# Kernel optimization log

Measured on AMD Instinct MI355X. Metric: run time of the kernel, lower is better.

The kernel has to match this reference:

```python
import jax, jax.numpy as jnp
import numpy as np

B, IN_CAPS, IN_DIM = 64, 2048, 16
NUM_CAPS, DIM_CAPS = 32, 16
NUM_ROUTING = 3
EPS = 1e-7


def squash(s):
    # squash along last (capsule vector) dim: ||s||^2/(1+||s||^2) * s/||s||
    sq_norm = jnp.sum(s * s, axis=-1, keepdims=True)
    scale = sq_norm / (1.0 + sq_norm) / jnp.sqrt(sq_norm + EPS)
    return scale * s


def setup_inputs() -> dict:
    key = jax.random.key(0)
    k1, k2 = jax.random.split(key)
    inputs = jax.random.normal(k1, (B, IN_CAPS, IN_DIM), dtype=jnp.float32)
    # original code inits xavier then overwrites with uniform(-1, 1)
    W = jax.random.uniform(k2, (IN_CAPS, NUM_CAPS, IN_DIM, DIM_CAPS),
                           dtype=jnp.float32, minval=-1.0, maxval=1.0)
    return {"inputs": inputs, "W": W}


def reference(inputs, W):
    # inputs_hat: [b, i(in_caps), j(num_caps), m(dim_caps)]
    inputs_hat = jnp.einsum('ijnm,bin->bijm', W, inputs)
    b = jnp.zeros((inputs.shape[0], IN_CAPS, NUM_CAPS), dtype=inputs.dtype)
    outputs = None
    for i in range(NUM_ROUTING):
        c = jax.nn.softmax(b, axis=1)                      # over input capsules
        outputs = squash(jnp.einsum('bij,bijm->bjm', c, inputs_hat))
        if i < NUM_ROUTING - 1:
            b = b + jnp.einsum('bjm,bijm->bij', outputs, inputs_hat)
    return outputs
```

## Files before the change

kernel.cpp:

```cpp
#include <hip/hip_runtime.h>
#include <hip/hip_fp16.h>
#include <math.h>

#define BATCH    64
#define IN_CAPS  2048
#define IN_DIM   16
#define NUM_CAPS 32
#define DIM_CAPS 16
#define NROUTE   3
#define CAPS_EPS 1e-7f

typedef unsigned short ushort_t;

__global__ __launch_bounds__(256) void caps_hat_kernel(
    const float* __restrict__ x, const float* __restrict__ W,
    ushort_t* __restrict__ hat)
{
  const int bid   = blockIdx.x;
  const int ig    = bid & 127;
  const int jb    = bid >> 7;
  const int t     = threadIdx.x;
  const int wv    = t >> 6;
  const int l     = t & 63;
  const int j     = jb * 4 + wv;
  const int i_loc = l >> 2;
  const int m0    = (l & 3) * 4;
  const int i     = ig * 16 + i_loc;

  float4 Wr[16];
  {
    const float* wbase = W + (((size_t)i * NUM_CAPS + j) * IN_DIM) * DIM_CAPS + m0;
#pragma unroll
    for (int n = 0; n < 16; ++n)
      Wr[n] = *reinterpret_cast<const float4*>(wbase + n * DIM_CAPS);
  }

  __shared__ float xs[16][16][17];

  for (int bc = 0; bc < 4; ++bc) {
    const int b0 = bc * 16;
#pragma unroll
    for (int k = 0; k < 4; ++k) {
      const int u   = t + k * 256;
      const int bl  = u >> 6;
      const int rem = u & 63;
      const int il  = rem >> 2;
      const int n0  = (rem & 3) * 4;
      float4 v = *reinterpret_cast<const float4*>(
          x + ((size_t)(b0 + bl) * IN_CAPS + ig * 16 + il) * IN_DIM + n0);
      xs[bl][il][n0 + 0] = v.x;
      xs[bl][il][n0 + 1] = v.y;
      xs[bl][il][n0 + 2] = v.z;
      xs[bl][il][n0 + 3] = v.w;
    }
    __syncthreads();
#pragma unroll
    for (int bl = 0; bl < 16; ++bl) {
      const int b = b0 + bl;
      float4 acc = make_float4(0.f, 0.f, 0.f, 0.f);
#pragma unroll
      for (int n = 0; n < 16; ++n) {
        const float xv = xs[bl][i_loc][n];
        acc.x = fmaf(Wr[n].x, xv, acc.x);
        acc.y = fmaf(Wr[n].y, xv, acc.y);
        acc.z = fmaf(Wr[n].z, xv, acc.z);
        acc.w = fmaf(Wr[n].w, xv, acc.w);
      }
      ushort4 st;
      st.x = __half_as_ushort(__float2half(acc.x));
      st.y = __half_as_ushort(__float2half(acc.y));
      st.z = __half_as_ushort(__float2half(acc.z));
      st.w = __half_as_ushort(__float2half(acc.w));
      *reinterpret_cast<ushort4*>(
          hat + (((size_t)b * NUM_CAPS + j) * IN_CAPS + i) * DIM_CAPS + m0) = st;
    }
    __syncthreads();
  }
}

__global__ __launch_bounds__(512) void caps_route_kernel(
    const ushort_t* __restrict__ hat, float* __restrict__ out)
{
  __shared__ float red[8][20];
  __shared__ float outs[16];

  const int bid  = blockIdx.x;
  const int t    = threadIdx.x;
  const int lane = t & 63;
  const int wv   = t >> 6;
  const int mh   = t & 1;

  const ushort_t* base = hat + (size_t)bid * (IN_CAPS * DIM_CAPS);

  uint4 g[8];
#pragma unroll
  for (int q = 0; q < 8; ++q)
    g[q] = *reinterpret_cast<const uint4*>(base + (size_t)(t + 512 * q) * 8);

#define HVAL(q, s) __half2float(__ushort_as_half((ushort_t)( \
    ((s) & 1) ? (((const unsigned int*)&g[(q)])[(s) >> 1] >> 16) \
              : (((const unsigned int*)&g[(q)])[(s) >> 1] & 0xffffu))))

  const int b1 = (lane >> 1) & 1;
  const int b2 = (lane >> 2) & 1;
  const int b3 = (lane >> 3) & 1;
  const int m_fin = 8 * mh + 4 * b3 + 2 * b2 + b1;

  float lg[8];
#pragma unroll
  for (int q = 0; q < 8; ++q) lg[q] = 0.f;

  for (int r = 0; r < NROUTE; ++r) {
    float e[8];
    float Ep = 0.f;
    if (r == 0) {
#pragma unroll
      for (int q = 0; q < 8; ++q) e[q] = 1.f;
    } else {
#pragma unroll
      for (int q = 0; q < 8; ++q) { e[q] = __expf(lg[q]); Ep += e[q]; }
    }

    float acc[8];
#pragma unroll
    for (int s = 0; s < 8; ++s) {
      float a = 0.f;
#pragma unroll
      for (int q = 0; q < 8; ++q) a = fmaf(e[q], HVAL(q, s), a);
      acc[s] = a;
    }

    float v4[4];
#pragma unroll
    for (int k = 0; k < 4; ++k) {
      float send = b1 ? acc[2 * k] : acc[2 * k + 1];
      float recv = __shfl_xor(send, 2);
      float keep = b1 ? acc[2 * k + 1] : acc[2 * k];
      v4[k] = keep + recv;
    }
    float v2[2];
#pragma unroll
    for (int k = 0; k < 2; ++k) {
      float send = b2 ? v4[2 * k] : v4[2 * k + 1];
      float recv = __shfl_xor(send, 4);
      float keep = b2 ? v4[2 * k + 1] : v4[2 * k];
      v2[k] = keep + recv;
    }
    float z;
    {
      float send = b3 ? v2[0] : v2[1];
      float recv = __shfl_xor(send, 8);
      float keep = b3 ? v2[1] : v2[0];
      z = keep + recv;
    }
    z += __shfl_xor(z, 16);
    z += __shfl_xor(z, 32);

    if (r > 0) {
      Ep += __shfl_xor(Ep, 2);
      Ep += __shfl_xor(Ep, 4);
      Ep += __shfl_xor(Ep, 8);
      Ep += __shfl_xor(Ep, 16);
      Ep += __shfl_xor(Ep, 32);
      if (lane == 16) red[wv][16] = Ep;
    }
    if (lane < 16) red[wv][m_fin] = z;
    __syncthreads();

    if (t < 16) {
      float s = 0.f;
#pragma unroll
      for (int w = 0; w < 8; ++w) s += red[w][t];
      float E;
      if (r == 0) E = (float)IN_CAPS;
      else {
        E = 0.f;
#pragma unroll
        for (int w = 0; w < 8; ++w) E += red[w][16];
      }
      float sm = s / E;
      float n2 = sm * sm;
#pragma unroll
      for (int off = 8; off >= 1; off >>= 1) n2 += __shfl_xor(n2, off);
      const float scale = n2 / (1.0f + n2) * rsqrtf(n2 + CAPS_EPS);
      const float o = scale * sm;
      outs[t] = o;
      if (r == NROUTE - 1)
        out[(size_t)bid * DIM_CAPS + t] = o;
    }
    __syncthreads();

    if (r < NROUTE - 1) {
#pragma unroll
      for (int q = 0; q < 8; ++q) {
        float d = 0.f;
#pragma unroll
        for (int s = 0; s < 8; ++s) d = fmaf(outs[8 * mh + s], HVAL(q, s), d);
        d += __shfl_xor(d, 1);
        lg[q] += d;
      }
    }
  }
#undef HVAL
}

extern "C" void kernel_launch(void* const* d_in, const int* in_sizes, int n_in,
                              void* d_out, int out_size, void* d_ws, size_t ws_size,
                              hipStream_t stream) {
  (void)in_sizes; (void)n_in; (void)out_size; (void)ws_size;
  const float* x = (const float*)d_in[0];
  const float* W = (const float*)d_in[1];
  float* outp = (float*)d_out;
  ushort_t* hat = (ushort_t*)d_ws;

  caps_hat_kernel<<<dim3(1024), dim3(256), 0, stream>>>(x, W, hat);
  caps_route_kernel<<<dim3(BATCH * NUM_CAPS), dim3(512), 0, stream>>>(hat, outp);
}
```

Measured before the change: 79.03 us.

## Split hat kernel batch across grid y and vectorize shared-memory x reads

The hat kernel grid doubles, with each block handling half the batch (32 instead of 64). This gives more blocks for occupancy and load balance, at the cost of loading each W tile twice. The shared x tile is padded to 20 floats so float4 stores and loads are aligned. The inner product now reads x as float4 from LDS instead of scalar reads.

```diff
diff --git a/kernel.cpp b/kernel.cpp
--- a/kernel.cpp
+++ b/kernel.cpp
@@ -19,6 +19,7 @@
   const int bid   = blockIdx.x;
   const int ig    = bid & 127;
   const int jb    = bid >> 7;
+  const int bhalf = blockIdx.y;
   const int t     = threadIdx.x;
   const int wv    = t >> 6;
   const int l     = t & 63;
@@ -35,10 +36,10 @@
       Wr[n] = *reinterpret_cast<const float4*>(wbase + n * DIM_CAPS);
   }
 
-  __shared__ float xs[16][16][17];
-
-  for (int bc = 0; bc < 4; ++bc) {
-    const int b0 = bc * 16;
+  __shared__ float xs[16][16][20];
+
+  for (int bc = 0; bc < 2; ++bc) {
+    const int b0 = bhalf * 32 + bc * 16;
 #pragma unroll
     for (int k = 0; k < 4; ++k) {
       const int u   = t + k * 256;
@@ -48,10 +49,7 @@
       const int n0  = (rem & 3) * 4;
       float4 v = *reinterpret_cast<const float4*>(
           x + ((size_t)(b0 + bl) * IN_CAPS + ig * 16 + il) * IN_DIM + n0);
-      xs[bl][il][n0 + 0] = v.x;
-      xs[bl][il][n0 + 1] = v.y;
-      xs[bl][il][n0 + 2] = v.z;
-      xs[bl][il][n0 + 3] = v.w;
+      *reinterpret_cast<float4*>(&xs[bl][il][n0]) = v;
     }
     __syncthreads();
 #pragma unroll
@@ -59,12 +57,24 @@
       const int b = b0 + bl;
       float4 acc = make_float4(0.f, 0.f, 0.f, 0.f);
 #pragma unroll
-      for (int n = 0; n < 16; ++n) {
-        const float xv = xs[bl][i_loc][n];
-        acc.x = fmaf(Wr[n].x, xv, acc.x);
-        acc.y = fmaf(Wr[n].y, xv, acc.y);
-        acc.z = fmaf(Wr[n].z, xv, acc.z);
-        acc.w = fmaf(Wr[n].w, xv, acc.w);
+      for (int nb = 0; nb < 4; ++nb) {
+        const float4 xv = *reinterpret_cast<const float4*>(&xs[bl][i_loc][nb * 4]);
+        acc.x = fmaf(Wr[4 * nb + 0].x, xv.x, acc.x);
+        acc.y = fmaf(Wr[4 * nb + 0].y, xv.x, acc.y);
+        acc.z = fmaf(Wr[4 * nb + 0].z, xv.x, acc.z);
+        acc.w = fmaf(Wr[4 * nb + 0].w, xv.x, acc.w);
+        acc.x = fmaf(Wr[4 * nb + 1].x, xv.y, acc.x);
+        acc.y = fmaf(Wr[4 * nb + 1].y, xv.y, acc.y);
+        acc.z = fmaf(Wr[4 * nb + 1].z, xv.y, acc.z);
+        acc.w = fmaf(Wr[4 * nb + 1].w, xv.y, acc.w);
+        acc.x = fmaf(Wr[4 * nb + 2].x, xv.z, acc.x);
+        acc.y = fmaf(Wr[4 * nb + 2].y, xv.z, acc.y);
+        acc.z = fmaf(Wr[4 * nb + 2].z, xv.z, acc.z);
+        acc.w = fmaf(Wr[4 * nb + 2].w, xv.z, acc.w);
+        acc.x = fmaf(Wr[4 * nb + 3].x, xv.w, acc.x);
+        acc.y = fmaf(Wr[4 * nb + 3].y, xv.w, acc.y);
+        acc.z = fmaf(Wr[4 * nb + 3].z, xv.w, acc.z);
+        acc.w = fmaf(Wr[4 * nb + 3].w, xv.w, acc.w);
       }
       ushort4 st;
       st.x = __half_as_ushort(__float2half(acc.x));
@@ -213,6 +223,6 @@
   float* outp = (float*)d_out;
   ushort_t* hat = (ushort_t*)d_ws;
 
-  caps_hat_kernel<<<dim3(1024), dim3(256), 0, stream>>>(x, W, hat);
+  caps_hat_kernel<<<dim3(1024, 2), dim3(256), 0, stream>>>(x, W, hat);
   caps_route_kernel<<<dim3(BATCH * NUM_CAPS), dim3(512), 0, stream>>>(hat, outp);
 }
```

Result: slower. 85.38 us (+8.0%).
